# Optimization experiments

Measured on AMD Instinct MI355X. Metric: run time of the kernel, lower is better.

Reference implementation:

```python
import math
import jax, jax.numpy as jnp
import numpy as np

B, L, S, H, E, D = 2, 2048, 2048, 16, 64, 64

def setup_inputs() -> dict:
    key = jax.random.key(0)
    k1, k2, k3, k4, k5 = jax.random.split(key, 5)
    return {
        "queries": jax.random.normal(k1, (B, L, H, E), dtype=jnp.float32),
        "keys": jax.random.normal(k2, (B, S, H, E), dtype=jnp.float32),
        "values": jax.random.normal(k3, (B, S, H, D), dtype=jnp.float32),
        "tau": jax.random.uniform(k4, (B, 1), dtype=jnp.float32),
        "delta": jax.random.normal(k5, (B, S), dtype=jnp.float32),
        "attn_mask": jnp.zeros((1,), dtype=jnp.bool_),
    }

def reference(queries, keys, values, tau, delta, attn_mask):
    # queries: [B,L,H,E], keys: [B,S,H,E], values: [B,S,H,D]
    # tau: [B,1] -> [B,1,1,1]; delta: [B,S] -> [B,1,1,S]
    # mask_flag=False, so attn_mask is unused. Dropout is identity at eval.
    E_ = queries.shape[-1]
    scale = 1.0 / math.sqrt(E_)
    scores = jnp.einsum('blhe,bshe->bhls', queries, keys)  # [B,H,L,S]
    scores = scores * tau[:, None, None, :]                # de-stationary scale
    scores = scores + delta[:, None, None, :]              # de-stationary shift
    A = jax.nn.softmax(scale * scores, axis=-1)            # [B,H,L,S]
    V = jnp.einsum('bhls,bshd->blhd', A, values)           # [B,L,H,D]
    return V
```

## Files before the change

### kernel.cpp

```cpp
#include <hip/hip_runtime.h>


#define Bb 2
#define Ll 2048
#define Ss 2048
#define Hh 16
#define Ee 64
#define Dd 64
#define KV 64
#define NT 16

typedef _Float16 f16x8 __attribute__((ext_vector_type(8)));
typedef _Float16 f16x4 __attribute__((ext_vector_type(4)));
typedef __fp16 fp16x2 __attribute__((ext_vector_type(2)));
typedef float f32x4 __attribute__((ext_vector_type(4)));

union Pk2 { fp16x2 h; unsigned u; };
union PackU { unsigned u[4]; f16x8 v; };

#define GLDS(gp, lp) __builtin_amdgcn_global_load_lds( \
    (const __attribute__((address_space(1))) void*)(gp), \
    (__attribute__((address_space(3))) void*)(lp), 16, 0, 0)

#if __has_builtin(__builtin_amdgcn_exp2f)
#define EXP2(x) __builtin_amdgcn_exp2f(x)
#else
#define EXP2(x) exp2f(x)
#endif

#define LOG2E 1.4426950408889634f

__global__ __launch_bounds__(256)
void prepass_k(const float* __restrict__ K, _Float16* __restrict__ K16,
               const float* __restrict__ delta, float* __restrict__ delta2)
{
    const unsigned v = blockIdx.x * 256 + threadIdx.x;
    const unsigned e4 = v & 15;
    const unsigned h  = (v >> 4) & 15;
    const unsigned s  = (v >> 8) & (Ss - 1);
    const unsigned b  = v >> 19;
    const f32x4 src = ((const f32x4*)K)[v];
    f16x4 t;
    t[0] = (_Float16)src[0]; t[1] = (_Float16)src[1];
    t[2] = (_Float16)src[2]; t[3] = (_Float16)src[3];
    ((f16x4*)K16)[(((size_t)(b * Hh + h) * Ss + s) * 16) + e4] = t;
    if (v < (Bb * Ss) / 4) {
        const float sc = 0.125f * LOG2E;
        f32x4 dd = ((const f32x4*)delta)[v];
        ((f32x4*)delta2)[v] = (f32x4){sc * dd[0], sc * dd[1], sc * dd[2], sc * dd[3]};
    }
}

__global__ __launch_bounds__(256)
void prepass_v(const float* __restrict__ V, _Float16* __restrict__ VT16)
{
    __shared__ _Float16 TL[64][66];
    const int tid  = threadIdx.x;
    const int wave = tid >> 6;
    const int lane = tid & 63;
    const int bh = blockIdx.y;
    const int b  = bh >> 4;
    const int h  = bh & 15;
    const int s0 = blockIdx.x * 64;

    #pragma unroll
    for (int rr = 0; rr < 16; ++rr) {
        const int row = wave * 16 + rr;
        TL[row][lane] = (_Float16)V[((size_t)(b * Ss + s0 + row) * Hh + h) * Dd + lane];
    }
    __syncthreads();
    const int d  = tid >> 2;
    const int sq = (tid & 3) * 16;
    union { _Float16 h[16]; f16x8 v[2]; } tmp;
    #pragma unroll
    for (int i = 0; i < 16; ++i) tmp.h[i] = TL[sq + i][d];
    f16x8* dp = (f16x8*)(VT16 + ((size_t)(b * Hh + h) * Dd + d) * Ss + s0 + sq);
    dp[0] = tmp.v[0];
    dp[1] = tmp.v[1];
}


#define PBODY(T, CP, CN, DP, DN)                                                     \
{                                                                                    \
    const int sb_ = sBase + (T) * KV;                                                \
    if ((T) + 2 < NT) {                                                              \
        unsigned char* kw = stBase + ((T) & 1) * 8192 + wq * 1024;                   \
        GLDS(kb + (size_t)(sb_ + 2 * KV + row0) * 128 + slotS * 16, kw);             \
        GLDS(kb + (size_t)(sb_ + 2 * KV + row0 + 32) * 128 + slotS * 16, kw + 4096); \
    }                                                                                \
    if ((T) + 1 < NT) {                                                              \
        unsigned char* vw = stBase + 16384 + (((T) + 1) & 1) * 8192 + wq * 1024;     \
        GLDS(vtb + (size_t)row0 * (Ss * 2) + (sb_ + KV) * 2 + slotS * 16, vw);       \
        GLDS(vtb + (size_t)(row0 + 32) * (Ss * 2) + (sb_ + KV) * 2 + slotS * 16, vw + 4096); \
        _Pragma("unroll")                                                            \
        for (int q4 = 0; q4 < 4; ++q4)                                               \
            DN[q4] = *(const f32x4*)(d2b + sb_ + KV + q4 * 16 + 4 * g);              \
        const unsigned char* Ksm = stBase + (((T) + 1) & 1) * 8192;                  \
        _Pragma("unroll")                                                            \
        for (int qg = 0; qg < 2; ++qg)                                               \
            _Pragma("unroll")                                                        \
            for (int t4 = 0; t4 < 4; ++t4)                                           \
                CN[qg][t4] = (f32x4){0.f, 0.f, 0.f, 0.f};                            \
        __builtin_amdgcn_s_setprio(1);                                               \
        _Pragma("unroll")                                                            \
        for (int t4 = 0; t4 < 4; ++t4) {                                             \
            const int srow = t4 * 16 + lq;                                           \
            _Pragma("unroll")                                                        \
            for (int es = 0; es < 2; ++es) {                                         \
                const int slot = (es * 4 + g) ^ (srow & 7);                          \
                f16x8 ak = *(const f16x8*)(Ksm + srow * 128 + slot * 16);            \
                CN[0][t4] = __builtin_amdgcn_mfma_f32_16x16x32_f16(ak, aq[0][es], CN[0][t4], 0, 0, 0); \
                CN[1][t4] = __builtin_amdgcn_mfma_f32_16x16x32_f16(ak, aq[1][es], CN[1][t4], 0, 0, 0); \
            }                                                                        \
        }                                                                            \
        __builtin_amdgcn_s_setprio(0);                                               \
    }                                                                                \
    PackU bp[2][2];                                                                  \
    _Pragma("unroll")                                                                \
    for (int qg = 0; qg < 2; ++qg) {                                                 \
        float p[16];                                                                 \
        float tmax = -1e30f;                                                         \
        _Pragma("unroll")                                                            \
        for (int t4 = 0; t4 < 4; ++t4)                                               \
            _Pragma("unroll")                                                        \
            for (int j = 0; j < 4; ++j) {                                            \
                float z = fmaf(alpha2, CP[qg][t4][j], DP[t4][j]);                    \
                p[t4 * 4 + j] = z;                                                   \
                tmax = fmaxf(tmax, z);                                               \
            }                                                                        \
        if (!__all(tmax <= m_run[qg] + 11.5416f)) {                                  \
            float rmax = fmaxf(tmax, __shfl_xor(tmax, 16));                          \
            rmax = fmaxf(rmax, __shfl_xor(rmax, 32));                                \
            const float m_new = fmaxf(m_run[qg], rmax);                              \
            const float corr = EXP2(m_run[qg] - m_new);                              \
            l_run[qg] *= corr;                                                       \
            _Pragma("unroll")                                                        \
            for (int dt = 0; dt < 4; ++dt)                                           \
                _Pragma("unroll")                                                    \
                for (int j = 0; j < 4; ++j) osum[qg][dt][j] *= corr;                 \
            m_run[qg] = m_new;                                                       \
        }                                                                            \
        float psum = 0.f;                                                            \
        _Pragma("unroll")                                                            \
        for (int i = 0; i < 16; ++i) { p[i] = EXP2(p[i] - m_run[qg]); psum += p[i]; } \
        l_run[qg] += psum;                                                           \
        unsigned pk[8];                                                              \
        _Pragma("unroll")                                                            \
        for (int t4 = 0; t4 < 4; ++t4) {                                             \
            Pk2 u0, u1;                                                              \
            u0.h = __builtin_amdgcn_cvt_pkrtz(p[4 * t4], p[4 * t4 + 1]);             \
            u1.h = __builtin_amdgcn_cvt_pkrtz(p[4 * t4 + 2], p[4 * t4 + 3]);         \
            pk[t4 * 2] = u0.u;                                                       \
            pk[t4 * 2 + 1] = u1.u;                                                   \
        }                                                                            \
        _Pragma("unroll")                                                            \
        for (int ks = 0; ks < 2; ++ks) {                                             \
            unsigned a0 = __shfl(pk[ks * 4 + 0], srcA), a1 = __shfl(pk[ks * 4 + 1], srcA); \
            unsigned a2 = __shfl(pk[ks * 4 + 2], srcA), a3 = __shfl(pk[ks * 4 + 3], srcA); \
            unsigned b0 = __shfl(pk[ks * 4 + 0], srcB), b1 = __shfl(pk[ks * 4 + 1], srcB); \
            unsigned b2 = __shfl(pk[ks * 4 + 2], srcB), b3 = __shfl(pk[ks * 4 + 3], srcB); \
            bp[qg][ks].u[0] = gh ? a2 : a0;                                          \
            bp[qg][ks].u[1] = gh ? a3 : a1;                                          \
            bp[qg][ks].u[2] = gh ? b2 : b0;                                          \
            bp[qg][ks].u[3] = gh ? b3 : b1;                                          \
        }                                                                            \
    }                                                                                \
    {                                                                                \
        const unsigned char* Vsm = stBase + 16384 + ((T) & 1) * 8192;                \
        __builtin_amdgcn_s_setprio(1);                                               \
        _Pragma("unroll")                                                            \
        for (int ks = 0; ks < 2; ++ks)                                               \
            _Pragma("unroll")                                                        \
            for (int dt = 0; dt < 4; ++dt) {                                         \
                const int vrow = dt * 16 + lq;                                       \
                const int slot = (ks * 4 + g) ^ (vrow & 7);                          \
                f16x8 av = *(const f16x8*)(Vsm + vrow * 128 + slot * 16);            \
                osum[0][dt] = __builtin_amdgcn_mfma_f32_16x16x32_f16(av, bp[0][ks].v, osum[0][dt], 0, 0, 0); \
                osum[1][dt] = __builtin_amdgcn_mfma_f32_16x16x32_f16(av, bp[1][ks].v, osum[1][dt], 0, 0, 0); \
            }                                                                        \
        __builtin_amdgcn_s_setprio(0);                                               \
    }                                                                                \
    __syncthreads();                                                                 \
}

__global__ __launch_bounds__(512)
void dsattn_fwd_v8(const float* __restrict__ Q, const _Float16* __restrict__ K16,
                   const _Float16* __restrict__ VT16, const float* __restrict__ tau,
                   const float* __restrict__ delta2, float* __restrict__ out)
{
    extern __shared__ __align__(16) unsigned char smem[];

    const int tid  = threadIdx.x;
    const int wave = tid >> 6;
    const int half = wave >> 2;
    const int wq   = wave & 3;
    const int lane = tid & 63;
    const int lq   = lane & 15;
    const int g    = lane >> 4;
    const int tid_h = tid & 255;

    const int bid = blockIdx.x;
    const int xcd = bid & 7;
    const int kk  = bid >> 3;
    const int bh  = xcd * 4 + (kk & 3);
    const int b   = bh >> 4;
    const int h   = bh & 15;
    const int q0  = (kk >> 2) * 128;
    const int qw  = q0 + wq * 32;

    const float alpha2 = 0.125f * LOG2E * tau[b];

    f16x8 aq[2][2];
    #pragma unroll
    for (int qg = 0; qg < 2; ++qg) {
        const float* qp = Q + (((size_t)b * Ll + qw + qg * 16 + lq) * Hh + h) * Ee;
        #pragma unroll
        for (int es = 0; es < 2; ++es) {
            const float* p = qp + es * 32 + g * 8;
            f16x8 t;
            #pragma unroll
            for (int j = 0; j < 8; ++j) t[j] = (_Float16)p[j];
            aq[qg][es] = t;
        }
    }

    f32x4 osum[2][4];
    #pragma unroll
    for (int qg = 0; qg < 2; ++qg)
        #pragma unroll
        for (int i = 0; i < 4; ++i) osum[qg][i] = (f32x4){0.f, 0.f, 0.f, 0.f};
    float m_run[2] = {-1e30f, -1e30f};
    float l_run[2] = {0.0f, 0.0f};

    const unsigned char* kb  = (const unsigned char*)(K16 + (size_t)(b * Hh + h) * Ss * Ee);
    const unsigned char* vtb = (const unsigned char*)(VT16 + (size_t)(b * Hh + h) * Dd * Ss);
    const float* d2b = delta2 + (size_t)b * Ss;

    const int row0  = tid_h >> 3;
    const int slotS = (tid_h & 7) ^ (row0 & 7);
    unsigned char* stBase = smem + half * 32768;
    const int sBase = half * (Ss / 2);

    const int srcA = lq + 32 * (g & 1);
    const int srcB = srcA + 16;
    const bool gh = (g >> 1);

    {
        unsigned char* kw0 = stBase + wq * 1024;
        GLDS(kb + (size_t)(sBase + row0) * 128 + slotS * 16, kw0);
        GLDS(kb + (size_t)(sBase + row0 + 32) * 128 + slotS * 16, kw0 + 4096);
        unsigned char* vw0 = stBase + 16384 + wq * 1024;
        GLDS(vtb + (size_t)row0 * (Ss * 2) + sBase * 2 + slotS * 16, vw0);
        GLDS(vtb + (size_t)(row0 + 32) * (Ss * 2) + sBase * 2 + slotS * 16, vw0 + 4096);
        unsigned char* kw1 = stBase + 8192 + wq * 1024;
        GLDS(kb + (size_t)(sBase + KV + row0) * 128 + slotS * 16, kw1);
        GLDS(kb + (size_t)(sBase + KV + row0 + 32) * 128 + slotS * 16, kw1 + 4096);
    }
    f32x4 dA[4], dB[4];
    #pragma unroll
    for (int q4 = 0; q4 < 4; ++q4)
        dA[q4] = *(const f32x4*)(d2b + sBase + q4 * 16 + 4 * g);
    __syncthreads();

    f32x4 cA[2][4], cB[2][4];
    #pragma unroll
    for (int qg = 0; qg < 2; ++qg)
        #pragma unroll
        for (int t4 = 0; t4 < 4; ++t4) cA[qg][t4] = (f32x4){0.f, 0.f, 0.f, 0.f};
    {
        const unsigned char* Ksm = stBase;
        #pragma unroll
        for (int t4 = 0; t4 < 4; ++t4) {
            const int srow = t4 * 16 + lq;
            #pragma unroll
            for (int es = 0; es < 2; ++es) {
                const int slot = (es * 4 + g) ^ (srow & 7);
                f16x8 ak = *(const f16x8*)(Ksm + srow * 128 + slot * 16);
                cA[0][t4] = __builtin_amdgcn_mfma_f32_16x16x32_f16(ak, aq[0][es], cA[0][t4], 0, 0, 0);
                cA[1][t4] = __builtin_amdgcn_mfma_f32_16x16x32_f16(ak, aq[1][es], cA[1][t4], 0, 0, 0);
            }
        }
    }
    __syncthreads();

    for (int t = 0; t < NT; t += 2) {
        PBODY(t,     cA, cB, dA, dB);
        PBODY(t + 1, cB, cA, dB, dA);
    }

    #pragma unroll
    for (int qg = 0; qg < 2; ++qg) {
        float l = l_run[qg];
        l += __shfl_xor(l, 16);
        l += __shfl_xor(l, 32);
        l_run[qg] = l;
    }

    float (*Part)[2][16][68] = (float (*)[2][16][68])smem;
    if (half == 1) {
        #pragma unroll
        for (int qg = 0; qg < 2; ++qg) {
            #pragma unroll
            for (int dt = 0; dt < 4; ++dt)
                *(f32x4*)&Part[wq][qg][lq][dt * 16 + 4 * g] = osum[qg][dt];
            if (g == 0) {
                Part[wq][qg][lq][64] = m_run[qg];
                Part[wq][qg][lq][65] = l_run[qg];
            }
        }
    }
    __syncthreads();
    if (half == 0) {
        #pragma unroll
        for (int qg = 0; qg < 2; ++qg) {
            const float m1 = Part[wq][qg][lq][64];
            const float l1 = Part[wq][qg][lq][65];
            const float m  = fmaxf(m_run[qg], m1);
            const float s0 = EXP2(m_run[qg] - m);
            const float s1 = EXP2(m1 - m);
            const float inv = 1.0f / (l_run[qg] * s0 + l1 * s1);
            #pragma unroll
            for (int dt = 0; dt < 4; ++dt) {
                f32x4 p1 = *(const f32x4*)&Part[wq][qg][lq][dt * 16 + 4 * g];
                #pragma unroll
                for (int j = 0; j < 4; ++j)
                    osum[qg][dt][j] = (osum[qg][dt][j] * s0 + p1[j] * s1) * inv;
            }
        }
    }
    __syncthreads();
    float (*Osm)[68] = (float (*)[68])smem;
    if (half == 0) {
        #pragma unroll
        for (int qg = 0; qg < 2; ++qg)
            #pragma unroll
            for (int dt = 0; dt < 4; ++dt)
                *(f32x4*)&Osm[wq * 32 + qg * 16 + lq][dt * 16 + 4 * g] = osum[qg][dt];
    }
    __syncthreads();
    {
        float* ob = out + (((size_t)b * Ll + q0) * Hh + h) * Dd;
        #pragma unroll
        for (int i = 0; i < 16; ++i) {
            const int r = wave * 16 + i;
            ob[(size_t)r * (Hh * Dd) + lane] = Osm[r][lane];
        }
    }
}

__global__ __launch_bounds__(256)
void dsattn_fwd(const float* __restrict__ Q, const float* __restrict__ K,
                const float* __restrict__ V, const float* __restrict__ tau,
                const float* __restrict__ delta, float* __restrict__ out)
{
    __shared__ __align__(16) unsigned char Ksm[32 * 128];
    __shared__ __align__(16) unsigned char VTsm[64 * 80];
    __shared__ float dsm[32];
    __shared__ float Osm[4][16][68];

    const int tid  = threadIdx.x;
    const int wave = tid >> 6;
    const int lane = tid & 63;
    const int lq   = lane & 15;
    const int g    = lane >> 4;

    const int bh = blockIdx.y;
    const int b  = bh >> 4;
    const int h  = bh & 15;
    const int q0 = blockIdx.x * 64;

    const float alpha = 0.125f * tau[b];

    f16x8 aq[2];
    {
        const float* qp = Q + (((long)b * Ll + q0 + wave * 16 + lq) * Hh + h) * Ee;
        #pragma unroll
        for (int es = 0; es < 2; ++es) {
            const float* p = qp + es * 32 + g * 8;
            f16x8 t;
            #pragma unroll
            for (int j = 0; j < 8; ++j) t[j] = (_Float16)p[j];
            aq[es] = t;
        }
    }

    f32x4 osum[4];
    #pragma unroll
    for (int i = 0; i < 4; ++i) osum[i] = (f32x4){0.f, 0.f, 0.f, 0.f};
    float m_run = -1e30f, l_run = 0.0f;

    const float* kb = K + ((long)b * Ss * Hh + h) * Ee;
    const float* vb = V + ((long)b * Ss * Hh + h) * Dd;
    const float* db = delta + (long)b * Ss;

    const int kr    = tid >> 3;
    const int kc    = (tid & 7) * 8;
    const int kslot = (((tid & 7) ^ (kr & 7)) * 16);
    const int vd    = tid & 63;
    const int vsh   = tid >> 6;

    for (int sb = 0; sb < Ss; sb += 32) {
        __syncthreads();
        {
            const float* src = kb + (long)(sb + kr) * (Hh * Ee) + kc;
            f16x8 t;
            #pragma unroll
            for (int j = 0; j < 8; ++j) t[j] = (_Float16)src[j];
            *(f16x8*)(Ksm + kr * 128 + kslot) = t;
        }
        {
            const float* src = vb + (long)(sb + vsh * 8) * (Hh * Dd) + vd;
            f16x8 t;
            #pragma unroll
            for (int j = 0; j < 8; ++j) t[j] = (_Float16)src[j * (Hh * Dd)];
            *(f16x8*)(VTsm + vd * 80 + vsh * 16) = t;
        }
        if (tid < 32) dsm[tid] = 0.125f * db[sb + tid];
        __syncthreads();

        float p[8];
        float tmax = -1e30f;
        #pragma unroll
        for (int t = 0; t < 2; ++t) {
            f32x4 c = (f32x4){0.f, 0.f, 0.f, 0.f};
            #pragma unroll
            for (int es = 0; es < 2; ++es) {
                const int srow = t * 16 + lq;
                const int slot = ((es * 4 + g) ^ (srow & 7)) * 16;
                f16x8 ak = *(const f16x8*)(Ksm + srow * 128 + slot);
                c = __builtin_amdgcn_mfma_f32_16x16x32_f16(ak, aq[es], c, 0, 0, 0);
            }
            #pragma unroll
            for (int j = 0; j < 4; ++j) {
                float z = alpha * c[j] + dsm[t * 16 + 4 * g + j];
                p[t * 4 + j] = z;
                tmax = fmaxf(tmax, z);
            }
        }
        tmax = fmaxf(tmax, __shfl_xor(tmax, 16));
        tmax = fmaxf(tmax, __shfl_xor(tmax, 32));
        const float m_new = fmaxf(m_run, tmax);
        const float corr  = __expf(m_run - m_new);
        float psum = 0.f;
        #pragma unroll
        for (int i = 0; i < 8; ++i) { p[i] = __expf(p[i] - m_new); psum += p[i]; }
        psum += __shfl_xor(psum, 16);
        psum += __shfl_xor(psum, 32);
        l_run = l_run * corr + psum;
        m_run = m_new;
        #pragma unroll
        for (int dt = 0; dt < 4; ++dt)
            #pragma unroll
            for (int j = 0; j < 4; ++j)
                osum[dt][j] *= corr;

        Pk2 u00, u01, u10, u11;
        u00.h = __builtin_amdgcn_cvt_pkrtz(p[0], p[1]);
        u01.h = __builtin_amdgcn_cvt_pkrtz(p[2], p[3]);
        u10.h = __builtin_amdgcn_cvt_pkrtz(p[4], p[5]);
        u11.h = __builtin_amdgcn_cvt_pkrtz(p[6], p[7]);
        const int srcA = lq + 32 * (g & 1);
        const int srcB = srcA + 16;
        unsigned a00 = __shfl(u00.u, srcA), a01 = __shfl(u01.u, srcA);
        unsigned a10 = __shfl(u10.u, srcA), a11 = __shfl(u11.u, srcA);
        unsigned b00 = __shfl(u00.u, srcB), b01 = __shfl(u01.u, srcB);
        unsigned b10 = __shfl(u10.u, srcB), b11 = __shfl(u11.u, srcB);
        const bool hi = (g >= 2);
        PackU bp;
        bp.u[0] = hi ? a10 : a00;
        bp.u[1] = hi ? a11 : a01;
        bp.u[2] = hi ? b10 : b00;
        bp.u[3] = hi ? b11 : b01;

        #pragma unroll
        for (int dt = 0; dt < 4; ++dt) {
            f16x8 av = *(const f16x8*)(VTsm + (dt * 16 + lq) * 80 + g * 16);
            osum[dt] = __builtin_amdgcn_mfma_f32_16x16x32_f16(av, bp.v, osum[dt], 0, 0, 0);
        }
    }

    const float inv = 1.0f / l_run;
    #pragma unroll
    for (int dt = 0; dt < 4; ++dt)
        #pragma unroll
        for (int j = 0; j < 4; ++j)
            Osm[wave][lq][dt * 16 + 4 * g + j] = osum[dt][j] * inv;
    __syncthreads();
    {
        float* ob = out + (((long)b * Ll + q0 + wave * 16) * Hh + h) * Dd;
        #pragma unroll
        for (int r = 0; r < 16; ++r)
            ob[(long)r * (Hh * Dd) + lane] = Osm[wave][r][lane];
    }
}

extern "C" void kernel_launch(void* const* d_in, const int* in_sizes, int n_in,
                              void* d_out, int out_size, void* d_ws, size_t ws_size,
                              hipStream_t stream) {
    const float* Q     = (const float*)d_in[0];
    const float* K     = (const float*)d_in[1];
    const float* V     = (const float*)d_in[2];
    const float* tau   = (const float*)d_in[3];
    const float* delta = (const float*)d_in[4];
    float* out = (float*)d_out;

    const size_t elems = (size_t)Bb * Hh * Ss * Ee;
    const size_t need  = elems * 2 * 2 + (size_t)Bb * Ss * 4;

    if (ws_size >= need) {
        _Float16* K16    = (_Float16*)d_ws;
        _Float16* VT16   = K16 + elems;
        float*    delta2 = (float*)(VT16 + elems);
        hipLaunchKernelGGL(prepass_k, dim3(elems / 4 / 256), dim3(256), 0, stream,
                           K, K16, delta, delta2);
        hipLaunchKernelGGL(prepass_v, dim3(Ss / 64, Bb * Hh), dim3(256), 0, stream, V, VT16);
        hipLaunchKernelGGL(dsattn_fwd_v8, dim3(512), dim3(512), 65536, stream,
                           Q, K16, VT16, tau, delta2, out);
    } else {
        hipLaunchKernelGGL(dsattn_fwd, dim3(Ll / 64, Bb * Hh), dim3(256), 0, stream,
                           Q, K, V, tau, delta, out);
    }
}
```

Baseline: 86.96 us.

## Drop split-KV halves and two-query-group waves; use 64-row blocks of 4 waves

Replaces the 512-thread block (two halves each walking half of the key range, with a shared-memory merge of partial softmax states) with a 256-thread block where each wave owns 16 query rows and walks the full key range. The grid doubles to 1024 blocks with half the shared memory, which removes the cross-half merge and its extra barriers and reduces per-thread registers. The cost is that each wave no longer reuses one K/V tile across two query groups, so more tile loads are issued per unit of work. The row max and row sum are also rewritten as balanced trees.

Result: slower. 100.6 us (+15.6%).

```diff
diff --git a/kernel.cpp b/kernel.cpp
--- a/kernel.cpp
+++ b/kernel.cpp
@@ -8,7 +8,7 @@
 #define Ee 64
 #define Dd 64
 #define KV 64
-#define NT 16
+#define NT 32
 
 typedef _Float16 f16x8 __attribute__((ext_vector_type(8)));
 typedef _Float16 f16x4 __attribute__((ext_vector_type(4)));
@@ -82,25 +82,22 @@
 
 #define PBODY(T, CP, CN, DP, DN)                                                     \
 {                                                                                    \
-    const int sb_ = sBase + (T) * KV;                                                \
+    const int sb_ = (T) * KV;                                                        \
     if ((T) + 2 < NT) {                                                              \
-        unsigned char* kw = stBase + ((T) & 1) * 8192 + wq * 1024;                   \
+        unsigned char* kw = smem + ((T) & 1) * 8192 + wave * 1024;                   \
         GLDS(kb + (size_t)(sb_ + 2 * KV + row0) * 128 + slotS * 16, kw);             \
         GLDS(kb + (size_t)(sb_ + 2 * KV + row0 + 32) * 128 + slotS * 16, kw + 4096); \
     }                                                                                \
     if ((T) + 1 < NT) {                                                              \
-        unsigned char* vw = stBase + 16384 + (((T) + 1) & 1) * 8192 + wq * 1024;     \
+        unsigned char* vw = smem + 16384 + (((T) + 1) & 1) * 8192 + wave * 1024;     \
         GLDS(vtb + (size_t)row0 * (Ss * 2) + (sb_ + KV) * 2 + slotS * 16, vw);       \
         GLDS(vtb + (size_t)(row0 + 32) * (Ss * 2) + (sb_ + KV) * 2 + slotS * 16, vw + 4096); \
         _Pragma("unroll")                                                            \
         for (int q4 = 0; q4 < 4; ++q4)                                               \
             DN[q4] = *(const f32x4*)(d2b + sb_ + KV + q4 * 16 + 4 * g);              \
-        const unsigned char* Ksm = stBase + (((T) + 1) & 1) * 8192;                  \
-        _Pragma("unroll")                                                            \
-        for (int qg = 0; qg < 2; ++qg)                                               \
-            _Pragma("unroll")                                                        \
-            for (int t4 = 0; t4 < 4; ++t4)                                           \
-                CN[qg][t4] = (f32x4){0.f, 0.f, 0.f, 0.f};                            \
+        const unsigned char* Ksm = smem + (((T) + 1) & 1) * 8192;                    \
+        _Pragma("unroll")                                                            \
+        for (int t4 = 0; t4 < 4; ++t4) CN[t4] = (f32x4){0.f, 0.f, 0.f, 0.f};         \
         __builtin_amdgcn_s_setprio(1);                                               \
         _Pragma("unroll")                                                            \
         for (int t4 = 0; t4 < 4; ++t4) {                                             \
@@ -109,64 +106,70 @@
             for (int es = 0; es < 2; ++es) {                                         \
                 const int slot = (es * 4 + g) ^ (srow & 7);                          \
                 f16x8 ak = *(const f16x8*)(Ksm + srow * 128 + slot * 16);            \
-                CN[0][t4] = __builtin_amdgcn_mfma_f32_16x16x32_f16(ak, aq[0][es], CN[0][t4], 0, 0, 0); \
-                CN[1][t4] = __builtin_amdgcn_mfma_f32_16x16x32_f16(ak, aq[1][es], CN[1][t4], 0, 0, 0); \
+                CN[t4] = __builtin_amdgcn_mfma_f32_16x16x32_f16(ak, aq[es], CN[t4], 0, 0, 0); \
             }                                                                        \
         }                                                                            \
         __builtin_amdgcn_s_setprio(0);                                               \
     }                                                                                \
-    PackU bp[2][2];                                                                  \
+    float p[16];                                                                     \
     _Pragma("unroll")                                                                \
-    for (int qg = 0; qg < 2; ++qg) {                                                 \
-        float p[16];                                                                 \
-        float tmax = -1e30f;                                                         \
-        _Pragma("unroll")                                                            \
-        for (int t4 = 0; t4 < 4; ++t4)                                               \
+    for (int t4 = 0; t4 < 4; ++t4)                                                   \
+        _Pragma("unroll")                                                            \
+        for (int j = 0; j < 4; ++j)                                                  \
+            p[t4 * 4 + j] = fmaf(alpha2, CP[t4][j], DP[t4][j]);                      \
+                                                             \
+    float x0 = fmaxf(p[0], p[1]),  x1 = fmaxf(p[2], p[3]);                           \
+    float x2 = fmaxf(p[4], p[5]),  x3 = fmaxf(p[6], p[7]);                           \
+    float x4 = fmaxf(p[8], p[9]),  x5 = fmaxf(p[10], p[11]);                         \
+    float x6 = fmaxf(p[12], p[13]), x7 = fmaxf(p[14], p[15]);                        \
+    x0 = fmaxf(x0, x1); x2 = fmaxf(x2, x3); x4 = fmaxf(x4, x5); x6 = fmaxf(x6, x7);  \
+    const float tmax = fmaxf(fmaxf(x0, x2), fmaxf(x4, x6));                          \
+    if (!__all(tmax <= m_run + 11.5416f)) {                                          \
+        float rmax = fmaxf(tmax, __shfl_xor(tmax, 16));                              \
+        rmax = fmaxf(rmax, __shfl_xor(rmax, 32));                                    \
+        const float m_new = fmaxf(m_run, rmax);                                      \
+        const float corr = EXP2(m_run - m_new);                                      \
+        l_run *= corr;                                                               \
+        _Pragma("unroll")                                                            \
+        for (int dt = 0; dt < 4; ++dt)                                               \
             _Pragma("unroll")                                                        \
-            for (int j = 0; j < 4; ++j) {                                            \
-                float z = fmaf(alpha2, CP[qg][t4][j], DP[t4][j]);                    \
-                p[t4 * 4 + j] = z;                                                   \
-                tmax = fmaxf(tmax, z);                                               \
-            }                                                                        \
-        if (!__all(tmax <= m_run[qg] + 11.5416f)) {                                  \
-            float rmax = fmaxf(tmax, __shfl_xor(tmax, 16));                          \
-            rmax = fmaxf(rmax, __shfl_xor(rmax, 32));                                \
-            const float m_new = fmaxf(m_run[qg], rmax);                              \
-            const float corr = EXP2(m_run[qg] - m_new);                              \
-            l_run[qg] *= corr;                                                       \
-            _Pragma("unroll")                                                        \
-            for (int dt = 0; dt < 4; ++dt)                                           \
-                _Pragma("unroll")                                                    \
-                for (int j = 0; j < 4; ++j) osum[qg][dt][j] *= corr;                 \
-            m_run[qg] = m_new;                                                       \
-        }                                                                            \
-        float psum = 0.f;                                                            \
-        _Pragma("unroll")                                                            \
-        for (int i = 0; i < 16; ++i) { p[i] = EXP2(p[i] - m_run[qg]); psum += p[i]; } \
-        l_run[qg] += psum;                                                           \
-        unsigned pk[8];                                                              \
-        _Pragma("unroll")                                                            \
-        for (int t4 = 0; t4 < 4; ++t4) {                                             \
-            Pk2 u0, u1;                                                              \
-            u0.h = __builtin_amdgcn_cvt_pkrtz(p[4 * t4], p[4 * t4 + 1]);             \
-            u1.h = __builtin_amdgcn_cvt_pkrtz(p[4 * t4 + 2], p[4 * t4 + 3]);         \
-            pk[t4 * 2] = u0.u;                                                       \
-            pk[t4 * 2 + 1] = u1.u;                                                   \
-        }                                                                            \
-        _Pragma("unroll")                                                            \
-        for (int ks = 0; ks < 2; ++ks) {                                             \
-            unsigned a0 = __shfl(pk[ks * 4 + 0], srcA), a1 = __shfl(pk[ks * 4 + 1], srcA); \
-            unsigned a2 = __shfl(pk[ks * 4 + 2], srcA), a3 = __shfl(pk[ks * 4 + 3], srcA); \
-            unsigned b0 = __shfl(pk[ks * 4 + 0], srcB), b1 = __shfl(pk[ks * 4 + 1], srcB); \
-            unsigned b2 = __shfl(pk[ks * 4 + 2], srcB), b3 = __shfl(pk[ks * 4 + 3], srcB); \
-            bp[qg][ks].u[0] = gh ? a2 : a0;                                          \
-            bp[qg][ks].u[1] = gh ? a3 : a1;                                          \
-            bp[qg][ks].u[2] = gh ? b2 : b0;                                          \
-            bp[qg][ks].u[3] = gh ? b3 : b1;                                          \
-        }                                                                            \
-    }                                                                                \
+            for (int j = 0; j < 4; ++j) osum[dt][j] *= corr;                         \
+        m_run = m_new;                                                               \
+    }                                                                                \
+    _Pragma("unroll")                                                                \
+    for (int i = 0; i < 16; ++i) p[i] = EXP2(p[i] - m_run);                          \
+                                                             \
     {                                                                                \
-        const unsigned char* Vsm = stBase + 16384 + ((T) & 1) * 8192;                \
+        float s0 = p[0] + p[1],  s1 = p[2] + p[3];                                   \
+        float s2 = p[4] + p[5],  s3 = p[6] + p[7];                                   \
+        float s4 = p[8] + p[9],  s5 = p[10] + p[11];                                 \
+        float s6 = p[12] + p[13], s7 = p[14] + p[15];                                \
+        s0 += s1; s2 += s3; s4 += s5; s6 += s7;                                      \
+        l_run += (s0 + s2) + (s4 + s6);                                              \
+    }                                                                                \
+    unsigned pk[8];                                                                  \
+    _Pragma("unroll")                                                                \
+    for (int t4 = 0; t4 < 4; ++t4) {                                                 \
+        Pk2 u0, u1;                                                                  \
+        u0.h = __builtin_amdgcn_cvt_pkrtz(p[4 * t4], p[4 * t4 + 1]);                 \
+        u1.h = __builtin_amdgcn_cvt_pkrtz(p[4 * t4 + 2], p[4 * t4 + 3]);             \
+        pk[t4 * 2] = u0.u;                                                           \
+        pk[t4 * 2 + 1] = u1.u;                                                       \
+    }                                                                                \
+    PackU bp[2];                                                                     \
+    _Pragma("unroll")                                                                \
+    for (int ks = 0; ks < 2; ++ks) {                                                 \
+        unsigned a0 = __shfl(pk[ks * 4 + 0], srcA), a1 = __shfl(pk[ks * 4 + 1], srcA); \
+        unsigned a2 = __shfl(pk[ks * 4 + 2], srcA), a3 = __shfl(pk[ks * 4 + 3], srcA); \
+        unsigned b0 = __shfl(pk[ks * 4 + 0], srcB), b1 = __shfl(pk[ks * 4 + 1], srcB); \
+        unsigned b2 = __shfl(pk[ks * 4 + 2], srcB), b3 = __shfl(pk[ks * 4 + 3], srcB); \
+        bp[ks].u[0] = gh ? a2 : a0;                                                  \
+        bp[ks].u[1] = gh ? a3 : a1;                                                  \
+        bp[ks].u[2] = gh ? b2 : b0;                                                  \
+        bp[ks].u[3] = gh ? b3 : b1;                                                  \
+    }                                                                                \
+    {                                                                                \
+        const unsigned char* Vsm = smem + 16384 + ((T) & 1) * 8192;                  \
         __builtin_amdgcn_s_setprio(1);                                               \
         _Pragma("unroll")                                                            \
         for (int ks = 0; ks < 2; ++ks)                                               \
@@ -175,16 +178,15 @@
                 const int vrow = dt * 16 + lq;                                       \
                 const int slot = (ks * 4 + g) ^ (vrow & 7);                          \
                 f16x8 av = *(const f16x8*)(Vsm + vrow * 128 + slot * 16);            \
-                osum[0][dt] = __builtin_amdgcn_mfma_f32_16x16x32_f16(av, bp[0][ks].v, osum[0][dt], 0, 0, 0); \
-                osum[1][dt] = __builtin_amdgcn_mfma_f32_16x16x32_f16(av, bp[1][ks].v, osum[1][dt], 0, 0, 0); \
+                osum[dt] = __builtin_amdgcn_mfma_f32_16x16x32_f16(av, bp[ks].v, osum[dt], 0, 0, 0); \
             }                                                                        \
         __builtin_amdgcn_s_setprio(0);                                               \
     }                                                                                \
     __syncthreads();                                                                 \
 }
 
-__global__ __launch_bounds__(512)
-void dsattn_fwd_v8(const float* __restrict__ Q, const _Float16* __restrict__ K16,
+__global__ __launch_bounds__(256)
+void dsattn_fwd_v9(const float* __restrict__ Q, const _Float16* __restrict__ K16,
                    const _Float16* __restrict__ VT16, const float* __restrict__ tau,
                    const float* __restrict__ delta2, float* __restrict__ out)
 {
@@ -192,12 +194,9 @@
 
     const int tid  = threadIdx.x;
     const int wave = tid >> 6;
-    const int half = wave >> 2;
-    const int wq   = wave & 3;
     const int lane = tid & 63;
     const int lq   = lane & 15;
     const int g    = lane >> 4;
-    const int tid_h = tid & 255;
 
     const int bid = blockIdx.x;
     const int xcd = bid & 7;
@@ -205,70 +204,63 @@
     const int bh  = xcd * 4 + (kk & 3);
     const int b   = bh >> 4;
     const int h   = bh & 15;
-    const int q0  = (kk >> 2) * 128;
-    const int qw  = q0 + wq * 32;
+    const int q0  = (kk >> 2) * 64;
+    const int qw  = q0 + wave * 16;
 
     const float alpha2 = 0.125f * LOG2E * tau[b];
 
-    f16x8 aq[2][2];
-    #pragma unroll
-    for (int qg = 0; qg < 2; ++qg) {
-        const float* qp = Q + (((size_t)b * Ll + qw + qg * 16 + lq) * Hh + h) * Ee;
+    f16x8 aq[2];
+    {
+        const float* qp = Q + (((size_t)b * Ll + qw + lq) * Hh + h) * Ee;
         #pragma unroll
         for (int es = 0; es < 2; ++es) {
             const float* p = qp + es * 32 + g * 8;
             f16x8 t;
             #pragma unroll
             for (int j = 0; j < 8; ++j) t[j] = (_Float16)p[j];
-            aq[qg][es] = t;
-        }
-    }
-
-    f32x4 osum[2][4];
-    #pragma unroll
-    for (int qg = 0; qg < 2; ++qg)
-        #pragma unroll
-        for (int i = 0; i < 4; ++i) osum[qg][i] = (f32x4){0.f, 0.f, 0.f, 0.f};
-    float m_run[2] = {-1e30f, -1e30f};
-    float l_run[2] = {0.0f, 0.0f};
+            aq[es] = t;
+        }
+    }
+
+    f32x4 osum[4];
+    #pragma unroll
+    for (int i = 0; i < 4; ++i) osum[i] = (f32x4){0.f, 0.f, 0.f, 0.f};
+    float m_run = -1e30f;
+    float l_run = 0.0f;
 
     const unsigned char* kb  = (const unsigned char*)(K16 + (size_t)(b * Hh + h) * Ss * Ee);
     const unsigned char* vtb = (const unsigned char*)(VT16 + (size_t)(b * Hh + h) * Dd * Ss);
     const float* d2b = delta2 + (size_t)b * Ss;
 
-    const int row0  = tid_h >> 3;
-    const int slotS = (tid_h & 7) ^ (row0 & 7);
-    unsigned char* stBase = smem + half * 32768;
-    const int sBase = half * (Ss / 2);
+    const int row0  = tid >> 3;
+    const int slotS = (tid & 7) ^ (row0 & 7);
 
     const int srcA = lq + 32 * (g & 1);
     const int srcB = srcA + 16;
     const bool gh = (g >> 1);
 
     {
-        unsigned char* kw0 = stBase + wq * 1024;
-        GLDS(kb + (size_t)(sBase + row0) * 128 + slotS * 16, kw0);
-        GLDS(kb + (size_t)(sBase + row0 + 32) * 128 + slotS * 16, kw0 + 4096);
-        unsigned char* vw0 = stBase + 16384 + wq * 1024;
-        GLDS(vtb + (size_t)row0 * (Ss * 2) + sBase * 2 + slotS * 16, vw0);
-        GLDS(vtb + (size_t)(row0 + 32) * (Ss * 2) + sBase * 2 + slotS * 16, vw0 + 4096);
-        unsigned char* kw1 = stBase + 8192 + wq * 1024;
-        GLDS(kb + (size_t)(sBase + KV + row0) * 128 + slotS * 16, kw1);
-        GLDS(kb + (size_t)(sBase + KV + row0 + 32) * 128 + slotS * 16, kw1 + 4096);
+        unsigned char* kw0 = smem + wave * 1024;
+        GLDS(kb + (size_t)row0 * 128 + slotS * 16, kw0);
+        GLDS(kb + (size_t)(row0 + 32) * 128 + slotS * 16, kw0 + 4096);
+        unsigned char* vw0 = smem + 16384 + wave * 1024;
+        GLDS(vtb + (size_t)row0 * (Ss * 2) + slotS * 16, vw0);
+        GLDS(vtb + (size_t)(row0 + 32) * (Ss * 2) + slotS * 16, vw0 + 4096);
+        unsigned char* kw1 = smem + 8192 + wave * 1024;
+        GLDS(kb + (size_t)(KV + row0) * 128 + slotS * 16, kw1);
+        GLDS(kb + (size_t)(KV + row0 + 32) * 128 + slotS * 16, kw1 + 4096);
     }
     f32x4 dA[4], dB[4];
     #pragma unroll
     for (int q4 = 0; q4 < 4; ++q4)
-        dA[q4] = *(const f32x4*)(d2b + sBase + q4 * 16 + 4 * g);
+        dA[q4] = *(const f32x4*)(d2b + q4 * 16 + 4 * g);
     __syncthreads();
 
-    f32x4 cA[2][4], cB[2][4];
-    #pragma unroll
-    for (int qg = 0; qg < 2; ++qg)
-        #pragma unroll
-        for (int t4 = 0; t4 < 4; ++t4) cA[qg][t4] = (f32x4){0.f, 0.f, 0.f, 0.f};
-    {
-        const unsigned char* Ksm = stBase;
+    f32x4 cA[4], cB[4];
+    #pragma unroll
+    for (int t4 = 0; t4 < 4; ++t4) cA[t4] = (f32x4){0.f, 0.f, 0.f, 0.f};
+    {
+        const unsigned char* Ksm = smem;
         #pragma unroll
         for (int t4 = 0; t4 < 4; ++t4) {
             const int srow = t4 * 16 + lq;
@@ -276,8 +268,7 @@
             for (int es = 0; es < 2; ++es) {
                 const int slot = (es * 4 + g) ^ (srow & 7);
                 f16x8 ak = *(const f16x8*)(Ksm + srow * 128 + slot * 16);
-                cA[0][t4] = __builtin_amdgcn_mfma_f32_16x16x32_f16(ak, aq[0][es], cA[0][t4], 0, 0, 0);
-                cA[1][t4] = __builtin_amdgcn_mfma_f32_16x16x32_f16(ak, aq[1][es], cA[1][t4], 0, 0, 0);
+                cA[t4] = __builtin_amdgcn_mfma_f32_16x16x32_f16(ak, aq[es], cA[t4], 0, 0, 0);
             }
         }
     }
@@ -288,55 +279,20 @@
         PBODY(t + 1, cB, cA, dB, dA);
     }
 
-    #pragma unroll
-    for (int qg = 0; qg < 2; ++qg) {
-        float l = l_run[qg];
+    {
+        float l = l_run;
         l += __shfl_xor(l, 16);
         l += __shfl_xor(l, 32);
-        l_run[qg] = l;
-    }
-
-    float (*Part)[2][16][68] = (float (*)[2][16][68])smem;
-    if (half == 1) {
-        #pragma unroll
-        for (int qg = 0; qg < 2; ++qg) {
-            #pragma unroll
-            for (int dt = 0; dt < 4; ++dt)
-                *(f32x4*)&Part[wq][qg][lq][dt * 16 + 4 * g] = osum[qg][dt];
-            if (g == 0) {
-                Part[wq][qg][lq][64] = m_run[qg];
-                Part[wq][qg][lq][65] = l_run[qg];
-            }
-        }
-    }
-    __syncthreads();
-    if (half == 0) {
-        #pragma unroll
-        for (int qg = 0; qg < 2; ++qg) {
-            const float m1 = Part[wq][qg][lq][64];
-            const float l1 = Part[wq][qg][lq][65];
-            const float m  = fmaxf(m_run[qg], m1);
-            const float s0 = EXP2(m_run[qg] - m);
-            const float s1 = EXP2(m1 - m);
-            const float inv = 1.0f / (l_run[qg] * s0 + l1 * s1);
-            #pragma unroll
-            for (int dt = 0; dt < 4; ++dt) {
-                f32x4 p1 = *(const f32x4*)&Part[wq][qg][lq][dt * 16 + 4 * g];
-                #pragma unroll
-                for (int j = 0; j < 4; ++j)
-                    osum[qg][dt][j] = (osum[qg][dt][j] * s0 + p1[j] * s1) * inv;
-            }
-        }
-    }
-    __syncthreads();
+        l_run = l;
+    }
+
     float (*Osm)[68] = (float (*)[68])smem;
-    if (half == 0) {
-        #pragma unroll
-        for (int qg = 0; qg < 2; ++qg)
-            #pragma unroll
-            for (int dt = 0; dt < 4; ++dt)
-                *(f32x4*)&Osm[wq * 32 + qg * 16 + lq][dt * 16 + 4 * g] = osum[qg][dt];
-    }
+    const float inv = 1.0f / l_run;
+    #pragma unroll
+    for (int dt = 0; dt < 4; ++dt)
+        #pragma unroll
+        for (int j = 0; j < 4; ++j)
+            Osm[wave * 16 + lq][dt * 16 + 4 * g + j] = osum[dt][j] * inv;
     __syncthreads();
     {
         float* ob = out + (((size_t)b * Ll + q0) * Hh + h) * Dd;
@@ -514,7 +470,7 @@
         hipLaunchKernelGGL(prepass_k, dim3(elems / 4 / 256), dim3(256), 0, stream,
                            K, K16, delta, delta2);
         hipLaunchKernelGGL(prepass_v, dim3(Ss / 64, Bb * Hh), dim3(256), 0, stream, V, VT16);
-        hipLaunchKernelGGL(dsattn_fwd_v8, dim3(512), dim3(512), 65536, stream,
+        hipLaunchKernelGGL(dsattn_fwd_v9, dim3(1024), dim3(256), 32768, stream,
                            Q, K16, VT16, tau, delta2, out);
     } else {
         hipLaunchKernelGGL(dsattn_fwd, dim3(Ll / 64, Bb * Hh), dim3(256), 0, stream,
```

## Switch attention main loop to 32x32x16 MFMA with permlane32 swap for P

Applied to the files above, without the earlier changes.

Rewrites the fused attention inner loop to use 32x32x16 f16 MFMA tiles instead of 16x16x32. With this layout a wave keeps one query row set, so the running max/sum reduction needs one cross-lane shuffle, and the P-to-B-operand reshuffle becomes two v_permlane32_swap instructions in place of many __shfl calls. Delta loads move to the start of each tile rather than being prefetched one tile ahead. The aim is fewer shuffle/LDS ops and denser matrix issue, at the cost of 32-wide accumulator register pressure and a reliance on the permlane32_swap instruction.

Result: faster. 81.35 us, median of 4 (-6.5%).

```diff
diff --git a/kernel.cpp b/kernel.cpp
--- a/kernel.cpp
+++ b/kernel.cpp
@@ -14,6 +14,7 @@
 typedef _Float16 f16x4 __attribute__((ext_vector_type(4)));
 typedef __fp16 fp16x2 __attribute__((ext_vector_type(2)));
 typedef float f32x4 __attribute__((ext_vector_type(4)));
+typedef float f32x16 __attribute__((ext_vector_type(16)));
 
 union Pk2 { fp16x2 h; unsigned u; };
 union PackU { unsigned u[4]; f16x8 v; };
@@ -29,6 +30,8 @@
 #endif
 
 #define LOG2E 1.4426950408889634f
+
+#define PSWAP(x, y) asm volatile("v_permlane32_swap_b32 %0, %1" : "+v"(x), "+v"(y))
 
 __global__ __launch_bounds__(256)
 void prepass_k(const float* __restrict__ K, _Float16* __restrict__ K16,
@@ -80,9 +83,16 @@
 }
 
 
-#define PBODY(T, CP, CN, DP, DN)                                                     \
+#define PBODY(T, CP, CN)                                                             \
 {                                                                                    \
     const int sb_ = sBase + (T) * KV;                                                \
+                                  \
+    f32x4 dreg[2][4];                                                                \
+    _Pragma("unroll")                                                                \
+    for (int st = 0; st < 2; ++st)                                                   \
+        _Pragma("unroll")                                                            \
+        for (int q4 = 0; q4 < 4; ++q4)                                               \
+            dreg[st][q4] = *(const f32x4*)(d2b + sb_ + st * 32 + q4 * 8 + hl * 4);   \
     if ((T) + 2 < NT) {                                                              \
         unsigned char* kw = stBase + ((T) & 1) * 8192 + wq * 1024;                   \
         GLDS(kb + (size_t)(sb_ + 2 * KV + row0) * 128 + slotS * 16, kw);             \
@@ -92,58 +102,61 @@
         unsigned char* vw = stBase + 16384 + (((T) + 1) & 1) * 8192 + wq * 1024;     \
         GLDS(vtb + (size_t)row0 * (Ss * 2) + (sb_ + KV) * 2 + slotS * 16, vw);       \
         GLDS(vtb + (size_t)(row0 + 32) * (Ss * 2) + (sb_ + KV) * 2 + slotS * 16, vw + 4096); \
-        _Pragma("unroll")                                                            \
-        for (int q4 = 0; q4 < 4; ++q4)                                               \
-            DN[q4] = *(const f32x4*)(d2b + sb_ + KV + q4 * 16 + 4 * g);              \
         const unsigned char* Ksm = stBase + (((T) + 1) & 1) * 8192;                  \
         _Pragma("unroll")                                                            \
-        for (int qg = 0; qg < 2; ++qg)                                               \
+        for (int st = 0; st < 2; ++st)                                               \
             _Pragma("unroll")                                                        \
-            for (int t4 = 0; t4 < 4; ++t4)                                           \
-                CN[qg][t4] = (f32x4){0.f, 0.f, 0.f, 0.f};                            \
+            for (int i = 0; i < 16; ++i) CN[st][i] = 0.f;                            \
         __builtin_amdgcn_s_setprio(1);                                               \
         _Pragma("unroll")                                                            \
-        for (int t4 = 0; t4 < 4; ++t4) {                                             \
-            const int srow = t4 * 16 + lq;                                           \
+        for (int st = 0; st < 2; ++st) {                                             \
+            const int krow = st * 32 + c31;                                          \
             _Pragma("unroll")                                                        \
-            for (int es = 0; es < 2; ++es) {                                         \
-                const int slot = (es * 4 + g) ^ (srow & 7);                          \
-                f16x8 ak = *(const f16x8*)(Ksm + srow * 128 + slot * 16);            \
-                CN[0][t4] = __builtin_amdgcn_mfma_f32_16x16x32_f16(ak, aq[0][es], CN[0][t4], 0, 0, 0); \
-                CN[1][t4] = __builtin_amdgcn_mfma_f32_16x16x32_f16(ak, aq[1][es], CN[1][t4], 0, 0, 0); \
+            for (int es = 0; es < 4; ++es) {                                         \
+                const int slot = (es * 2 + hl) ^ (krow & 7);                         \
+                f16x8 ak = *(const f16x8*)(Ksm + krow * 128 + slot * 16);            \
+                CN[st] = __builtin_amdgcn_mfma_f32_32x32x16_f16(ak, aq[es], CN[st], 0, 0, 0); \
             }                                                                        \
         }                                                                            \
         __builtin_amdgcn_s_setprio(0);                                               \
     }                                                                                \
-    PackU bp[2][2];                                                                  \
+    const unsigned char* Vsm = stBase + 16384 + ((T) & 1) * 8192;                    \
     _Pragma("unroll")                                                                \
-    for (int qg = 0; qg < 2; ++qg) {                                                 \
+    for (int st = 0; st < 2; ++st) {                                                 \
         float p[16];                                                                 \
-        float tmax = -1e30f;                                                         \
-        _Pragma("unroll")                                                            \
-        for (int t4 = 0; t4 < 4; ++t4)                                               \
+        _Pragma("unroll")                                                            \
+        for (int q4 = 0; q4 < 4; ++q4)                                               \
             _Pragma("unroll")                                                        \
-            for (int j = 0; j < 4; ++j) {                                            \
-                float z = fmaf(alpha2, CP[qg][t4][j], DP[t4][j]);                    \
-                p[t4 * 4 + j] = z;                                                   \
-                tmax = fmaxf(tmax, z);                                               \
-            }                                                                        \
-        if (!__all(tmax <= m_run[qg] + 11.5416f)) {                                  \
-            float rmax = fmaxf(tmax, __shfl_xor(tmax, 16));                          \
-            rmax = fmaxf(rmax, __shfl_xor(rmax, 32));                                \
-            const float m_new = fmaxf(m_run[qg], rmax);                              \
-            const float corr = EXP2(m_run[qg] - m_new);                              \
-            l_run[qg] *= corr;                                                       \
+            for (int j = 0; j < 4; ++j)                                              \
+                p[q4 * 4 + j] = fmaf(alpha2, CP[st][q4 * 4 + j], dreg[st][q4][j]);   \
+        float x0 = fmaxf(p[0], p[1]),  x1 = fmaxf(p[2], p[3]);                       \
+        float x2 = fmaxf(p[4], p[5]),  x3 = fmaxf(p[6], p[7]);                       \
+        float x4 = fmaxf(p[8], p[9]),  x5 = fmaxf(p[10], p[11]);                     \
+        float x6 = fmaxf(p[12], p[13]), x7 = fmaxf(p[14], p[15]);                    \
+        x0 = fmaxf(x0, x1); x2 = fmaxf(x2, x3); x4 = fmaxf(x4, x5); x6 = fmaxf(x6, x7); \
+        const float tmax = fmaxf(fmaxf(x0, x2), fmaxf(x4, x6));                      \
+        if (!__all(tmax <= m_run + 11.5416f)) {                                      \
+            float rmax = fmaxf(tmax, __shfl_xor(tmax, 32));                          \
+            const float m_new = fmaxf(m_run, rmax);                                  \
+            const float corr = EXP2(m_run - m_new);                                  \
+            l_run *= corr;                                                           \
             _Pragma("unroll")                                                        \
-            for (int dt = 0; dt < 4; ++dt)                                           \
+            for (int dt = 0; dt < 2; ++dt)                                           \
                 _Pragma("unroll")                                                    \
-                for (int j = 0; j < 4; ++j) osum[qg][dt][j] *= corr;                 \
-            m_run[qg] = m_new;                                                       \
+                for (int i = 0; i < 16; ++i) osum[dt][i] *= corr;                    \
+            m_run = m_new;                                                           \
         }                                                                            \
-        float psum = 0.f;                                                            \
-        _Pragma("unroll")                                                            \
-        for (int i = 0; i < 16; ++i) { p[i] = EXP2(p[i] - m_run[qg]); psum += p[i]; } \
-        l_run[qg] += psum;                                                           \
+        _Pragma("unroll")                                                            \
+        for (int i = 0; i < 16; ++i) p[i] = EXP2(p[i] - m_run);                      \
+        {                                                                            \
+            float s0 = p[0] + p[1],  s1 = p[2] + p[3];                               \
+            float s2 = p[4] + p[5],  s3 = p[6] + p[7];                               \
+            float s4 = p[8] + p[9],  s5 = p[10] + p[11];                             \
+            float s6 = p[12] + p[13], s7 = p[14] + p[15];                            \
+            s0 += s1; s2 += s3; s4 += s5; s6 += s7;                                  \
+            l_run += (s0 + s2) + (s4 + s6);                                          \
+        }                                                                            \
+            \
         unsigned pk[8];                                                              \
         _Pragma("unroll")                                                            \
         for (int t4 = 0; t4 < 4; ++t4) {                                             \
@@ -153,50 +166,42 @@
             pk[t4 * 2] = u0.u;                                                       \
             pk[t4 * 2 + 1] = u1.u;                                                   \
         }                                                                            \
+        __builtin_amdgcn_s_setprio(1);                                               \
         _Pragma("unroll")                                                            \
         for (int ks = 0; ks < 2; ++ks) {                                             \
-            unsigned a0 = __shfl(pk[ks * 4 + 0], srcA), a1 = __shfl(pk[ks * 4 + 1], srcA); \
-            unsigned a2 = __shfl(pk[ks * 4 + 2], srcA), a3 = __shfl(pk[ks * 4 + 3], srcA); \
-            unsigned b0 = __shfl(pk[ks * 4 + 0], srcB), b1 = __shfl(pk[ks * 4 + 1], srcB); \
-            unsigned b2 = __shfl(pk[ks * 4 + 2], srcB), b3 = __shfl(pk[ks * 4 + 3], srcB); \
-            bp[qg][ks].u[0] = gh ? a2 : a0;                                          \
-            bp[qg][ks].u[1] = gh ? a3 : a1;                                          \
-            bp[qg][ks].u[2] = gh ? b2 : b0;                                          \
-            bp[qg][ks].u[3] = gh ? b3 : b1;                                          \
+            unsigned b0 = pk[ks * 4 + 0], b1 = pk[ks * 4 + 1];                       \
+            unsigned b2 = pk[ks * 4 + 2], b3 = pk[ks * 4 + 3];                       \
+            PSWAP(b0, b2);                                                           \
+            PSWAP(b1, b3);                                                           \
+            PackU bf;                                                                \
+            bf.u[0] = b0; bf.u[1] = b1; bf.u[2] = b2; bf.u[3] = b3;                  \
+            _Pragma("unroll")                                                        \
+            for (int dt = 0; dt < 2; ++dt) {                                         \
+                const int vrow = dt * 32 + c31;                                      \
+                const int slot = (st * 4 + ks * 2 + hl) ^ (vrow & 7);                \
+                f16x8 av = *(const f16x8*)(Vsm + vrow * 128 + slot * 16);            \
+                osum[dt] = __builtin_amdgcn_mfma_f32_32x32x16_f16(av, bf.v, osum[dt], 0, 0, 0); \
+            }                                                                        \
         }                                                                            \
-    }                                                                                \
-    {                                                                                \
-        const unsigned char* Vsm = stBase + 16384 + ((T) & 1) * 8192;                \
-        __builtin_amdgcn_s_setprio(1);                                               \
-        _Pragma("unroll")                                                            \
-        for (int ks = 0; ks < 2; ++ks)                                               \
-            _Pragma("unroll")                                                        \
-            for (int dt = 0; dt < 4; ++dt) {                                         \
-                const int vrow = dt * 16 + lq;                                       \
-                const int slot = (ks * 4 + g) ^ (vrow & 7);                          \
-                f16x8 av = *(const f16x8*)(Vsm + vrow * 128 + slot * 16);            \
-                osum[0][dt] = __builtin_amdgcn_mfma_f32_16x16x32_f16(av, bp[0][ks].v, osum[0][dt], 0, 0, 0); \
-                osum[1][dt] = __builtin_amdgcn_mfma_f32_16x16x32_f16(av, bp[1][ks].v, osum[1][dt], 0, 0, 0); \
-            }                                                                        \
         __builtin_amdgcn_s_setprio(0);                                               \
     }                                                                                \
     __syncthreads();                                                                 \
 }
 
 __global__ __launch_bounds__(512)
-void dsattn_fwd_v8(const float* __restrict__ Q, const _Float16* __restrict__ K16,
-                   const _Float16* __restrict__ VT16, const float* __restrict__ tau,
-                   const float* __restrict__ delta2, float* __restrict__ out)
+void dsattn_fwd_v10(const float* __restrict__ Q, const _Float16* __restrict__ K16,
+                    const _Float16* __restrict__ VT16, const float* __restrict__ tau,
+                    const float* __restrict__ delta2, float* __restrict__ out)
 {
     extern __shared__ __align__(16) unsigned char smem[];
 
     const int tid  = threadIdx.x;
     const int wave = tid >> 6;
-    const int half = wave >> 2;
+    const int halfId = wave >> 2;
     const int wq   = wave & 3;
     const int lane = tid & 63;
-    const int lq   = lane & 15;
-    const int g    = lane >> 4;
+    const int c31  = lane & 31;
+    const int hl   = lane >> 5;
     const int tid_h = tid & 255;
 
     const int bid = blockIdx.x;
@@ -204,46 +209,41 @@
     const int kk  = bid >> 3;
     const int bh  = xcd * 4 + (kk & 3);
     const int b   = bh >> 4;
-    const int h   = bh & 15;
+    const int hd  = bh & 15;
     const int q0  = (kk >> 2) * 128;
     const int qw  = q0 + wq * 32;
 
     const float alpha2 = 0.125f * LOG2E * tau[b];
 
-    f16x8 aq[2][2];
+    f16x8 aq[4];
+    {
+        const float* qp = Q + (((size_t)b * Ll + qw + c31) * Hh + hd) * Ee;
+        #pragma unroll
+        for (int es = 0; es < 4; ++es) {
+            const float* p = qp + es * 16 + hl * 8;
+            f16x8 t;
+            #pragma unroll
+            for (int j = 0; j < 8; ++j) t[j] = (_Float16)p[j];
+            aq[es] = t;
+        }
+    }
+
+    f32x16 osum[2];
     #pragma unroll
-    for (int qg = 0; qg < 2; ++qg) {
-        const float* qp = Q + (((size_t)b * Ll + qw + qg * 16 + lq) * Hh + h) * Ee;
-        #pragma unroll
-        for (int es = 0; es < 2; ++es) {
-            const float* p = qp + es * 32 + g * 8;
-            f16x8 t;
-            #pragma unroll
-            for (int j = 0; j < 8; ++j) t[j] = (_Float16)p[j];
-            aq[qg][es] = t;
-        }
-    }
-
-    f32x4 osum[2][4];
-    #pragma unroll
-    for (int qg = 0; qg < 2; ++qg)
-        #pragma unroll
-        for (int i = 0; i < 4; ++i) osum[qg][i] = (f32x4){0.f, 0.f, 0.f, 0.f};
-    float m_run[2] = {-1e30f, -1e30f};
-    float l_run[2] = {0.0f, 0.0f};
-
-    const unsigned char* kb  = (const unsigned char*)(K16 + (size_t)(b * Hh + h) * Ss * Ee);
-    const unsigned char* vtb = (const unsigned char*)(VT16 + (size_t)(b * Hh + h) * Dd * Ss);
+    for (int dt = 0; dt < 2; ++dt)
+        #pragma unroll
+        for (int i = 0; i < 16; ++i) osum[dt][i] = 0.f;
+    float m_run = -1e30f;
+    float l_run = 0.0f;
+
+    const unsigned char* kb  = (const unsigned char*)(K16 + (size_t)(b * Hh + hd) * Ss * Ee);
+    const unsigned char* vtb = (const unsigned char*)(VT16 + (size_t)(b * Hh + hd) * Dd * Ss);
     const float* d2b = delta2 + (size_t)b * Ss;
 
     const int row0  = tid_h >> 3;
     const int slotS = (tid_h & 7) ^ (row0 & 7);
-    unsigned char* stBase = smem + half * 32768;
-    const int sBase = half * (Ss / 2);
-
-    const int srcA = lq + 32 * (g & 1);
-    const int srcB = srcA + 16;
-    const bool gh = (g >> 1);
+    unsigned char* stBase = smem + halfId * 32768;
+    const int sBase = halfId * (Ss / 2);
 
     {
         unsigned char* kw0 = stBase + wq * 1024;
@@ -256,90 +256,83 @@
         GLDS(kb + (size_t)(sBase + KV + row0) * 128 + slotS * 16, kw1);
         GLDS(kb + (size_t)(sBase + KV + row0 + 32) * 128 + slotS * 16, kw1 + 4096);
     }
-    f32x4 dA[4], dB[4];
+    __syncthreads();
+
+    f32x16 cA[2], cB[2];
     #pragma unroll
-    for (int q4 = 0; q4 < 4; ++q4)
-        dA[q4] = *(const f32x4*)(d2b + sBase + q4 * 16 + 4 * g);
-    __syncthreads();
-
-    f32x4 cA[2][4], cB[2][4];
-    #pragma unroll
-    for (int qg = 0; qg < 2; ++qg)
-        #pragma unroll
-        for (int t4 = 0; t4 < 4; ++t4) cA[qg][t4] = (f32x4){0.f, 0.f, 0.f, 0.f};
+    for (int st = 0; st < 2; ++st)
+        #pragma unroll
+        for (int i = 0; i < 16; ++i) cA[st][i] = 0.f;
     {
         const unsigned char* Ksm = stBase;
         #pragma unroll
-        for (int t4 = 0; t4 < 4; ++t4) {
-            const int srow = t4 * 16 + lq;
-            #pragma unroll
-            for (int es = 0; es < 2; ++es) {
-                const int slot = (es * 4 + g) ^ (srow & 7);
-                f16x8 ak = *(const f16x8*)(Ksm + srow * 128 + slot * 16);
-                cA[0][t4] = __builtin_amdgcn_mfma_f32_16x16x32_f16(ak, aq[0][es], cA[0][t4], 0, 0, 0);
-                cA[1][t4] = __builtin_amdgcn_mfma_f32_16x16x32_f16(ak, aq[1][es], cA[1][t4], 0, 0, 0);
+        for (int st = 0; st < 2; ++st) {
+            const int krow = st * 32 + c31;
+            #pragma unroll
+            for (int es = 0; es < 4; ++es) {
+                const int slot = (es * 2 + hl) ^ (krow & 7);
+                f16x8 ak = *(const f16x8*)(Ksm + krow * 128 + slot * 16);
+                cA[st] = __builtin_amdgcn_mfma_f32_32x32x16_f16(ak, aq[es], cA[st], 0, 0, 0);
             }
         }
     }
     __syncthreads();
 
     for (int t = 0; t < NT; t += 2) {
-        PBODY(t,     cA, cB, dA, dB);
-        PBODY(t + 1, cB, cA, dB, dA);
-    }
-
-    #pragma unroll
-    for (int qg = 0; qg < 2; ++qg) {
-        float l = l_run[qg];
-        l += __shfl_xor(l, 16);
-        l += __shfl_xor(l, 32);
-        l_run[qg] = l;
-    }
-
-    float (*Part)[2][16][68] = (float (*)[2][16][68])smem;
-    if (half == 1) {
-        #pragma unroll
-        for (int qg = 0; qg < 2; ++qg) {
-            #pragma unroll
-            for (int dt = 0; dt < 4; ++dt)
-                *(f32x4*)&Part[wq][qg][lq][dt * 16 + 4 * g] = osum[qg][dt];
-            if (g == 0) {
-                Part[wq][qg][lq][64] = m_run[qg];
-                Part[wq][qg][lq][65] = l_run[qg];
+        PBODY(t,     cA, cB);
+        PBODY(t + 1, cB, cA);
+    }
+
+    l_run += __shfl_xor(l_run, 32);
+
+    float (*Part)[32][68] = (float (*)[32][68])smem;
+    if (halfId == 1) {
+        #pragma unroll
+        for (int dt = 0; dt < 2; ++dt)
+            #pragma unroll
+            for (int q4 = 0; q4 < 4; ++q4) {
+                f32x4 v = (f32x4){osum[dt][q4 * 4], osum[dt][q4 * 4 + 1],
+                                  osum[dt][q4 * 4 + 2], osum[dt][q4 * 4 + 3]};
+                *(f32x4*)&Part[wq][c31][dt * 32 + q4 * 8 + hl * 4] = v;
             }
-        }
-    }
-    __syncthreads();
-    if (half == 0) {
-        #pragma unroll
-        for (int qg = 0; qg < 2; ++qg) {
-            const float m1 = Part[wq][qg][lq][64];
-            const float l1 = Part[wq][qg][lq][65];
-            const float m  = fmaxf(m_run[qg], m1);
-            const float s0 = EXP2(m_run[qg] - m);
-            const float s1 = EXP2(m1 - m);
-            const float inv = 1.0f / (l_run[qg] * s0 + l1 * s1);
-            #pragma unroll
-            for (int dt = 0; dt < 4; ++dt) {
-                f32x4 p1 = *(const f32x4*)&Part[wq][qg][lq][dt * 16 + 4 * g];
+        if (hl == 0) {
+            Part[wq][c31][64] = m_run;
+            Part[wq][c31][65] = l_run;
+        }
+    }
+    __syncthreads();
+    if (halfId == 0) {
+        const float m1 = Part[wq][c31][64];
+        const float l1 = Part[wq][c31][65];
+        const float m  = fmaxf(m_run, m1);
+        const float s0 = EXP2(m_run - m);
+        const float s1 = EXP2(m1 - m);
+        const float inv = 1.0f / (l_run * s0 + l1 * s1);
+        #pragma unroll
+        for (int dt = 0; dt < 2; ++dt)
+            #pragma unroll
+            for (int q4 = 0; q4 < 4; ++q4) {
+                f32x4 p1 = *(const f32x4*)&Part[wq][c31][dt * 32 + q4 * 8 + hl * 4];
                 #pragma unroll
                 for (int j = 0; j < 4; ++j)
-                    osum[qg][dt][j] = (osum[qg][dt][j] * s0 + p1[j] * s1) * inv;
+                    osum[dt][q4 * 4 + j] = (osum[dt][q4 * 4 + j] * s0 + p1[j] * s1) * inv;
             }
-        }
     }
     __syncthreads();
     float (*Osm)[68] = (float (*)[68])smem;
-    if (half == 0) {
-        #pragma unroll
-        for (int qg = 0; qg < 2; ++qg)
-            #pragma unroll
-            for (int dt = 0; dt < 4; ++dt)
-                *(f32x4*)&Osm[wq * 32 + qg * 16 + lq][dt * 16 + 4 * g] = osum[qg][dt];
+    if (halfId == 0) {
+        #pragma unroll
+        for (int dt = 0; dt < 2; ++dt)
+            #pragma unroll
+            for (int q4 = 0; q4 < 4; ++q4) {
+                f32x4 v = (f32x4){osum[dt][q4 * 4], osum[dt][q4 * 4 + 1],
+                                  osum[dt][q4 * 4 + 2], osum[dt][q4 * 4 + 3]};
+                *(f32x4*)&Osm[wq * 32 + c31][dt * 32 + q4 * 8 + hl * 4] = v;
+            }
     }
     __syncthreads();
     {
-        float* ob = out + (((size_t)b * Ll + q0) * Hh + h) * Dd;
+        float* ob = out + (((size_t)b * Ll + q0) * Hh + hd) * Dd;
         #pragma unroll
         for (int i = 0; i < 16; ++i) {
             const int r = wave * 16 + i;
@@ -514,7 +507,7 @@
         hipLaunchKernelGGL(prepass_k, dim3(elems / 4 / 256), dim3(256), 0, stream,
                            K, K16, delta, delta2);
         hipLaunchKernelGGL(prepass_v, dim3(Ss / 64, Bb * Hh), dim3(256), 0, stream, V, VT16);
-        hipLaunchKernelGGL(dsattn_fwd_v8, dim3(512), dim3(512), 65536, stream,
+        hipLaunchKernelGGL(dsattn_fwd_v10, dim3(512), dim3(512), 65536, stream,
                            Q, K16, VT16, tau, delta2, out);
     } else {
         hipLaunchKernelGGL(dsattn_fwd, dim3(Ll / 64, Bb * Hh), dim3(256), 0, stream,
```
